# Performance work log

Measured on AMD Instinct MI355X. Metric: run time of the kernel, lower is better.

## Reference

```python
import jax, jax.numpy as jnp
import numpy as np

N_NODES = 50000
N_EDGES = 640000
D_IN = 128
D_OUT = 128


def setup_inputs() -> dict:
    key = jax.random.key(0)
    k1, k2, k3, k4 = jax.random.split(key, 4)
    x = jax.random.normal(k1, (N_NODES, D_IN), dtype=jnp.float32)
    edge_index = jax.random.randint(k2, (2, N_EDGES), 0, N_NODES, dtype=jnp.int64)
    weight = jax.random.uniform(k3, (1,), dtype=jnp.float32)
    temperature = jnp.ones((1,), dtype=jnp.float32)
    W = jax.random.normal(k4, (D_IN, D_OUT), dtype=jnp.float32) * (1.0 / np.sqrt(D_IN))
    b = jnp.zeros((D_OUT,), dtype=jnp.float32)
    return {"x": x, "edge_index": edge_index, "weight": weight,
            "temperature": temperature, "W": W, "b": b}


def _gcn_conv(x, edge_index, W, b):
    N = x.shape[0]
    src, dst = edge_index[0], edge_index[1]
    loop = jnp.arange(N, dtype=edge_index.dtype)
    s = jnp.concatenate([src, loop])  # self-loops appended
    d = jnp.concatenate([dst, loop])
    deg = jax.ops.segment_sum(jnp.ones(s.shape[0], dtype=x.dtype), d, num_segments=N)
    dinv = jnp.where(deg > 0, deg ** -0.5, 0.0)
    norm = dinv[s] * dinv[d]  # [E+N]
    h = x @ W                 # linear transform first (PyG GCNConv)
    msg = h[s] * norm[:, None]
    out = jax.ops.segment_sum(msg, d, num_segments=N)
    return out + b


def _gradient_entropy(x, edge_index, temperature):
    # Boltzmann distribution over per-node Dirichlet energies;
    # entropy gradient w.r.t. node features (computed with autodiff).
    N = x.shape[0]
    src, dst = edge_index[0], edge_index[1]

    def entropy(z):
        diff = z[src] - z[dst]                                  # [E, D]
        E = jax.ops.segment_sum(jnp.sum(diff * diff, axis=-1), dst, num_segments=N)
        logp = jax.nn.log_softmax(-E / temperature[0])
        p = jnp.exp(logp)
        return -jnp.sum(p * logp)

    return jax.grad(entropy)(x)


def reference(x, edge_index, weight, temperature, W, b):
    h = _gcn_conv(x, edge_index, W, b)
    g = jax.lax.stop_gradient(_gradient_entropy(h, edge_index, temperature))
    return h + weight * g
```

## Files before the change

### kernel.cpp

```cpp
#include <hip/hip_runtime.h>

#define N_NODES 50000
#define N_EDGES 640000
#define NSCANB  196
#define MAXD    64

#define OFF_HTMPB    0
#define OFF_OBF      3200000
#define OFF_CURSOR   6400000
#define OFF_E        6450000
#define OFF_PMIN     6500000
#define OFF_PS0      6500256
#define OFF_PS1      6500512
#define OFF_WT       6500768
#define OFF_EBIN     6508960

typedef __attribute__((ext_vector_type(8))) short bf16x8;
typedef __attribute__((ext_vector_type(4))) float f32x4;

__device__ __forceinline__ unsigned short f2bf(float f) {
    unsigned u = __float_as_uint(f);
    unsigned r = u + 0x7fffu + ((u >> 16) & 1u);
    return (unsigned short)(r >> 16);
}
__device__ __forceinline__ float bflo(unsigned u) { return __uint_as_float(u << 16); }
__device__ __forceinline__ float bfhi(unsigned u) { return __uint_as_float(u & 0xffff0000u); }

__global__ __launch_bounds__(256) void k_init(const float* __restrict__ W,
                                              int* __restrict__ cursor,
                                              unsigned short* __restrict__ wtg) {
    int gtid = blockIdx.x * 256 + threadIdx.x;
    if (gtid < N_NODES) cursor[gtid] = 0;
    if (gtid < 4096) {
        int k = gtid >> 5, n4 = (gtid & 31) * 4;
        float4 v = *(const float4*)(W + k * 128 + n4);
        wtg[(n4 + 0) * 128 + k] = f2bf(v.x);
        wtg[(n4 + 1) * 128 + k] = f2bf(v.y);
        wtg[(n4 + 2) * 128 + k] = f2bf(v.z);
        wtg[(n4 + 3) * 128 + k] = f2bf(v.w);
    }
}

__global__ __launch_bounds__(256) void k_gemm(const float* __restrict__ x,
                                              const unsigned short* __restrict__ wtg,
                                              unsigned short* __restrict__ htmpb) {
    int tid = threadIdx.x;
    int wave = tid >> 6, lane = tid & 63, quad = lane >> 4, m16 = lane & 15;
    int r0 = blockIdx.x * 32 + (wave & 1) * 16;
    int ch = (wave >> 1) * 4;
    int arow = r0 + m16;
    int rowc = arow < N_NODES ? arow : N_NODES - 1;
    f32x4 acc[4];
    #pragma unroll
    for (int c = 0; c < 4; c++) acc[c] = (f32x4){0.f, 0.f, 0.f, 0.f};
    #pragma unroll
    for (int kt = 0; kt < 4; kt++) {
        int koff = kt * 32 + quad * 8;
        float4 xa = *(const float4*)(x + rowc * 128 + koff);
        float4 xb = *(const float4*)(x + rowc * 128 + koff + 4);
        bf16x8 af;
        af[0] = (short)f2bf(xa.x); af[1] = (short)f2bf(xa.y);
        af[2] = (short)f2bf(xa.z); af[3] = (short)f2bf(xa.w);
        af[4] = (short)f2bf(xb.x); af[5] = (short)f2bf(xb.y);
        af[6] = (short)f2bf(xb.z); af[7] = (short)f2bf(xb.w);
        #pragma unroll
        for (int c = 0; c < 4; c++) {
            bf16x8 bfrag = *(const bf16x8*)(wtg + ((ch + c) * 16 + m16) * 128 + koff);
            acc[c] = __builtin_amdgcn_mfma_f32_16x16x32_bf16(af, bfrag, acc[c], 0, 0, 0);
        }
    }
    #pragma unroll
    for (int reg = 0; reg < 4; reg++) {
        int grow = r0 + quad * 4 + reg;
        if (grow < N_NODES) {
            #pragma unroll
            for (int c = 0; c < 4; c++)
                htmpb[grow * 128 + (ch + c) * 16 + m16] = f2bf(acc[c][reg]);
        }
    }
}

__global__ __launch_bounds__(256) void k_bucket(const int* __restrict__ src,
                                                const int* __restrict__ dst,
                                                int* __restrict__ cursor,
                                                int* __restrict__ ebin) {
    int e = blockIdx.x * 256 + threadIdx.x;
    int d = dst[e];
    int pos = atomicAdd(&cursor[d], 1);
    if (pos < MAXD) ebin[d * MAXD + pos] = src[e];
}

__global__ __launch_bounds__(256) void k_gather(const unsigned short* __restrict__ htmpb,
                                                const int* __restrict__ deg,
                                                const float* __restrict__ b,
                                                const int* __restrict__ ebin,
                                                float* __restrict__ out,
                                                unsigned short* __restrict__ obf) {
    int node = blockIdx.x * 8 + (threadIdx.x >> 5);
    int lane = threadIdx.x & 31;
    int dg = deg[node]; if (dg > MAXD) dg = MAXD;
    float di = rsqrtf((float)(dg + 1));
    float4 bv = *(const float4*)(b + lane * 4);
    uint2 hv = *(const uint2*)(htmpb + node * 128 + lane * 4);
    float sl = di * di;
    float ax = bv.x + bflo(hv.x) * sl, ay = bv.y + bfhi(hv.x) * sl;
    float az = bv.z + bflo(hv.y) * sl, aw = bv.w + bfhi(hv.y) * sl;
    float cx = 0.f, cy = 0.f, cz = 0.f, cw = 0.f;
    const int* bin = ebin + node * MAXD;
    int k = 0;
    for (; k + 3 < dg; k += 4) {
        int s0 = bin[k], s1 = bin[k + 1], s2 = bin[k + 2], s3 = bin[k + 3];
        float n0 = di * rsqrtf((float)(deg[s0] + 1));
        float n1 = di * rsqrtf((float)(deg[s1] + 1));
        float n2 = di * rsqrtf((float)(deg[s2] + 1));
        float n3 = di * rsqrtf((float)(deg[s3] + 1));
        uint2 u0 = *(const uint2*)(htmpb + s0 * 128 + lane * 4);
        uint2 u1 = *(const uint2*)(htmpb + s1 * 128 + lane * 4);
        uint2 u2 = *(const uint2*)(htmpb + s2 * 128 + lane * 4);
        uint2 u3 = *(const uint2*)(htmpb + s3 * 128 + lane * 4);
        ax += bflo(u0.x) * n0; ay += bfhi(u0.x) * n0;
        az += bflo(u0.y) * n0; aw += bfhi(u0.y) * n0;
        cx += bflo(u1.x) * n1; cy += bfhi(u1.x) * n1;
        cz += bflo(u1.y) * n1; cw += bfhi(u1.y) * n1;
        ax += bflo(u2.x) * n2; ay += bfhi(u2.x) * n2;
        az += bflo(u2.y) * n2; aw += bfhi(u2.y) * n2;
        cx += bflo(u3.x) * n3; cy += bfhi(u3.x) * n3;
        cz += bflo(u3.y) * n3; cw += bfhi(u3.y) * n3;
    }
    for (; k < dg; k++) {
        int s0 = bin[k];
        float n0 = di * rsqrtf((float)(deg[s0] + 1));
        uint2 u0 = *(const uint2*)(htmpb + s0 * 128 + lane * 4);
        ax += bflo(u0.x) * n0; ay += bfhi(u0.x) * n0;
        az += bflo(u0.y) * n0; aw += bfhi(u0.y) * n0;
    }
    ax += cx; ay += cy; az += cz; aw += cw;
    *(float4*)(out + node * 128 + lane * 4) = make_float4(ax, ay, az, aw);
    uint2 pk;
    pk.x = (unsigned)f2bf(ax) | ((unsigned)f2bf(ay) << 16);
    pk.y = (unsigned)f2bf(az) | ((unsigned)f2bf(aw) << 16);
    *(uint2*)(obf + node * 128 + lane * 4) = pk;
}

__global__ __launch_bounds__(256) void k_energy(const unsigned short* __restrict__ obf,
                                                const int* __restrict__ deg,
                                                const int* __restrict__ ebin,
                                                float* __restrict__ E) {
    int node = blockIdx.x * 8 + (threadIdx.x >> 5);
    int lane = threadIdx.x & 31;
    int dg = deg[node]; if (dg > MAXD) dg = MAXD;
    uint2 ud = *(const uint2*)(obf + node * 128 + lane * 4);
    float o0 = bflo(ud.x), o1 = bfhi(ud.x), o2 = bflo(ud.y), o3 = bfhi(ud.y);
    float acc = 0.f, acc2 = 0.f;
    const int* bin = ebin + node * MAXD;
    int k = 0;
    for (; k + 3 < dg; k += 4) {
        int s0 = bin[k], s1 = bin[k + 1], s2 = bin[k + 2], s3 = bin[k + 3];
        uint2 a = *(const uint2*)(obf + s0 * 128 + lane * 4);
        uint2 c = *(const uint2*)(obf + s1 * 128 + lane * 4);
        uint2 g = *(const uint2*)(obf + s2 * 128 + lane * 4);
        uint2 h = *(const uint2*)(obf + s3 * 128 + lane * 4);
        float d0 = bflo(a.x) - o0, d1 = bfhi(a.x) - o1, d2 = bflo(a.y) - o2, d3 = bfhi(a.y) - o3;
        float e4 = bflo(c.x) - o0, e5 = bfhi(c.x) - o1, e6 = bflo(c.y) - o2, e7 = bfhi(c.y) - o3;
        float f0 = bflo(g.x) - o0, f1 = bfhi(g.x) - o1, f2 = bflo(g.y) - o2, f3 = bfhi(g.y) - o3;
        float h4 = bflo(h.x) - o0, h5 = bfhi(h.x) - o1, h6 = bflo(h.y) - o2, h7 = bfhi(h.y) - o3;
        acc  += d0 * d0 + d1 * d1 + d2 * d2 + d3 * d3;
        acc2 += e4 * e4 + e5 * e5 + e6 * e6 + e7 * e7;
        acc  += f0 * f0 + f1 * f1 + f2 * f2 + f3 * f3;
        acc2 += h4 * h4 + h5 * h5 + h6 * h6 + h7 * h7;
    }
    for (; k < dg; k++) {
        int s0 = bin[k];
        uint2 a = *(const uint2*)(obf + s0 * 128 + lane * 4);
        float d0 = bflo(a.x) - o0, d1 = bfhi(a.x) - o1, d2 = bflo(a.y) - o2, d3 = bfhi(a.y) - o3;
        acc += d0 * d0 + d1 * d1 + d2 * d2 + d3 * d3;
    }
    acc += acc2;
    #pragma unroll
    for (int off = 16; off; off >>= 1) acc += __shfl_xor(acc, off);
    if (lane == 0) E[node] = acc;
}

__global__ __launch_bounds__(256) void k_esoft(const float* __restrict__ E,
                                               const float* __restrict__ temp,
                                               float* __restrict__ pmin,
                                               float* __restrict__ ps0,
                                               float* __restrict__ ps1) {
    __shared__ float fred[12];
    int tid = threadIdx.x;
    int i = blockIdx.x * 256 + tid;
    int lane = tid & 63, wid = tid >> 6;
    float e = (i < N_NODES) ? E[i] : 3.402823466e38f;
    float m = e;
    #pragma unroll
    for (int off = 32; off; off >>= 1) m = fminf(m, __shfl_xor(m, off));
    if (lane == 0) fred[wid] = m;
    __syncthreads();
    float bm = fminf(fminf(fred[0], fred[1]), fminf(fred[2], fred[3]));
    float T = temp[0];
    float s0 = 0.f, s1 = 0.f;
    if (i < N_NODES) {
        float dd = (bm - e) / T;
        float ed = __expf(dd);
        s0 = ed; s1 = ed * dd;
    }
    #pragma unroll
    for (int off = 32; off; off >>= 1) { s0 += __shfl_xor(s0, off); s1 += __shfl_xor(s1, off); }
    __syncthreads();
    if (lane == 0) { fred[4 + wid] = s0; fred[8 + wid] = s1; }
    __syncthreads();
    if (tid == 0) {
        pmin[blockIdx.x] = bm;
        ps0[blockIdx.x] = fred[4] + fred[5] + fred[6] + fred[7];
        ps1[blockIdx.x] = fred[8] + fred[9] + fred[10] + fred[11];
    }
}

__global__ __launch_bounds__(256) void k_grad(const int* __restrict__ deg,
                                              const int* __restrict__ ebin,
                                              const float* __restrict__ E,
                                              const float* __restrict__ temp,
                                              const float* __restrict__ pmin,
                                              const float* __restrict__ ps0,
                                              const float* __restrict__ ps1,
                                              const float* __restrict__ weight,
                                              float* __restrict__ out) {
    __shared__ float fred[12];
    int tid = threadIdx.x;
    int lane = tid & 63, wid = tid >> 6;

    float pm = (tid < NSCANB) ? pmin[tid] : 3.402823466e38f;
    float m = pm;
    #pragma unroll
    for (int off = 32; off; off >>= 1) m = fminf(m, __shfl_xor(m, off));
    if (lane == 0) fred[wid] = m;
    __syncthreads();
    float gmin = fminf(fminf(fred[0], fred[1]), fminf(fred[2], fred[3]));
    float T = temp[0];
    float s0 = 0.f, s1 = 0.f;
    if (tid < NSCANB) {
        float dl = (gmin - pm) / T;
        float ex = __expf(dl);
        float b0 = ps0[tid], b1 = ps1[tid];
        s0 = ex * b0;
        s1 = ex * (b1 + dl * b0);
    }
    #pragma unroll
    for (int off = 32; off; off >>= 1) { s0 += __shfl_xor(s0, off); s1 += __shfl_xor(s1, off); }
    __syncthreads();
    if (lane == 0) { fred[4 + wid] = s0; fred[8 + wid] = s1; }
    __syncthreads();
    float S0 = fred[4] + fred[5] + fred[6] + fred[7];
    float S1 = fred[8] + fred[9] + fred[10] + fred[11];

    float wscale = 2.f * weight[0];
    int lane32 = tid & 31;
    int node = blockIdx.x * 8 + (tid >> 5);
    if (node >= N_NODES) return;
    float dd = (gmin - E[node]) / T;
    float qd = (__expf(dd) / S0) * (dd - S1 / S0) / T;
    if (qd == 0.f) return;
    float cc = wscale * qd;
    int dg = deg[node]; if (dg > MAXD) dg = MAXD;
    float4 od = *(const float4*)(out + node * 128 + lane32 * 4);
    float sx = 0.f, sy = 0.f, sz = 0.f, sw = 0.f;
    const int* bin = ebin + node * MAXD;
    for (int k = 0; k < dg; k++) {
        int s = bin[k];
        float4 a = *(const float4*)(out + s * 128 + lane32 * 4);
        float vx = cc * (a.x - od.x), vy = cc * (a.y - od.y);
        float vz = cc * (a.z - od.z), vw = cc * (a.w - od.w);
        float* os = out + s * 128 + lane32 * 4;
        atomicAdd(os + 0, vx); atomicAdd(os + 1, vy);
        atomicAdd(os + 2, vz); atomicAdd(os + 3, vw);
        sx += vx; sy += vy; sz += vz; sw += vw;
    }
    float* odp = out + node * 128 + lane32 * 4;
    atomicAdd(odp + 0, -sx); atomicAdd(odp + 1, -sy);
    atomicAdd(odp + 2, -sz); atomicAdd(odp + 3, -sw);
}

extern "C" void kernel_launch(void* const* d_in, const int* in_sizes, int n_in,
                              void* d_out, int out_size, void* d_ws, size_t ws_size,
                              hipStream_t stream) {
    const float* x      = (const float*)d_in[0];
    const int*   ei     = (const int*)d_in[1];
    const float* weight = (const float*)d_in[2];
    const float* temp   = (const float*)d_in[3];
    const float* W      = (const float*)d_in[4];
    const float* b      = (const float*)d_in[5];
    float* out = (float*)d_out;
    float* ws  = (float*)d_ws;

    const int* src = ei;
    const int* dst = ei + N_EDGES;

    unsigned short* htmpb = (unsigned short*)(ws + OFF_HTMPB);
    unsigned short* obf   = (unsigned short*)(ws + OFF_OBF);
    int*   cursor   = (int*)(ws + OFF_CURSOR);
    float* Earr     = ws + OFF_E;
    float* pminA    = ws + OFF_PMIN;
    float* ps0A     = ws + OFF_PS0;
    float* ps1A     = ws + OFF_PS1;
    unsigned short* wtg = (unsigned short*)(ws + OFF_WT);
    int*   ebin     = (int*)(ws + OFF_EBIN);

    k_init<<<NSCANB, 256, 0, stream>>>(W, cursor, wtg);
    k_gemm<<<1563, 256, 0, stream>>>(x, wtg, htmpb);
    k_bucket<<<N_EDGES / 256, 256, 0, stream>>>(src, dst, cursor, ebin);
    k_gather<<<6250, 256, 0, stream>>>(htmpb, cursor, b, ebin, out, obf);
    k_energy<<<6250, 256, 0, stream>>>(obf, cursor, ebin, Earr);
    k_esoft<<<NSCANB, 256, 0, stream>>>(Earr, temp, pminA, ps0A, ps1A);
    k_grad<<<6250, 256, 0, stream>>>(cursor, ebin, Earr, temp, pminA, ps0A, ps1A, weight, out);
}
```

Before: 218.1 us.

## Fold init into GEMM and fuse softmax statistics into persistent grad kernel

Removes the k_init kernel by zeroing the cursor and converting W to bf16 inside the GEMM, with each lane reading W columns directly (strided fp32 loads) instead of a pre-transposed bf16 copy. Removes k_esoft by having every block of k_grad redundantly compute the global min and online-softmax sums over all 50000 energies, and makes k_grad persistent with 781 blocks in a grid-stride loop. This saves two launches and the intermediate buffers, at the cost of redundant full-array scans per block, uncoalesced W reads in the GEMM, and fewer grad blocks to hide atomic latency.

```diff
diff --git a/kernel.cpp b/kernel.cpp
--- a/kernel.cpp
+++ b/kernel.cpp
@@ -2,18 +2,13 @@
 
 #define N_NODES 50000
 #define N_EDGES 640000
-#define NSCANB  196
 #define MAXD    64
 
 #define OFF_HTMPB    0
 #define OFF_OBF      3200000
 #define OFF_CURSOR   6400000
 #define OFF_E        6450000
-#define OFF_PMIN     6500000
-#define OFF_PS0      6500256
-#define OFF_PS1      6500512
-#define OFF_WT       6500768
-#define OFF_EBIN     6508960
+#define OFF_EBIN     6500000
 
 typedef __attribute__((ext_vector_type(8))) short bf16x8;
 typedef __attribute__((ext_vector_type(4))) float f32x4;
@@ -26,25 +21,14 @@
 __device__ __forceinline__ float bflo(unsigned u) { return __uint_as_float(u << 16); }
 __device__ __forceinline__ float bfhi(unsigned u) { return __uint_as_float(u & 0xffff0000u); }
 
-__global__ __launch_bounds__(256) void k_init(const float* __restrict__ W,
+__global__ __launch_bounds__(256) void k_gemm(const float* __restrict__ x,
+                                              const float* __restrict__ W,
                                               int* __restrict__ cursor,
-                                              unsigned short* __restrict__ wtg) {
-    int gtid = blockIdx.x * 256 + threadIdx.x;
-    if (gtid < N_NODES) cursor[gtid] = 0;
-    if (gtid < 4096) {
-        int k = gtid >> 5, n4 = (gtid & 31) * 4;
-        float4 v = *(const float4*)(W + k * 128 + n4);
-        wtg[(n4 + 0) * 128 + k] = f2bf(v.x);
-        wtg[(n4 + 1) * 128 + k] = f2bf(v.y);
-        wtg[(n4 + 2) * 128 + k] = f2bf(v.z);
-        wtg[(n4 + 3) * 128 + k] = f2bf(v.w);
-    }
-}
-
-__global__ __launch_bounds__(256) void k_gemm(const float* __restrict__ x,
-                                              const unsigned short* __restrict__ wtg,
                                               unsigned short* __restrict__ htmpb) {
     int tid = threadIdx.x;
+    int gtid = blockIdx.x * 256 + tid;
+    if (gtid < N_NODES) cursor[gtid] = 0;
+
     int wave = tid >> 6, lane = tid & 63, quad = lane >> 4, m16 = lane & 15;
     int r0 = blockIdx.x * 32 + (wave & 1) * 16;
     int ch = (wave >> 1) * 4;
@@ -65,7 +49,11 @@
         af[6] = (short)f2bf(xb.z); af[7] = (short)f2bf(xb.w);
         #pragma unroll
         for (int c = 0; c < 4; c++) {
-            bf16x8 bfrag = *(const bf16x8*)(wtg + ((ch + c) * 16 + m16) * 128 + koff);
+            int n = (ch + c) * 16 + m16;
+            bf16x8 bfrag;
+            #pragma unroll
+            for (int j = 0; j < 8; j++)
+                bfrag[j] = (short)f2bf(W[(koff + j) * 128 + n]);
             acc[c] = __builtin_amdgcn_mfma_f32_16x16x32_bf16(af, bfrag, acc[c], 0, 0, 0);
         }
     }
@@ -181,103 +169,82 @@
     if (lane == 0) E[node] = acc;
 }
 
-__global__ __launch_bounds__(256) void k_esoft(const float* __restrict__ E,
-                                               const float* __restrict__ temp,
-                                               float* __restrict__ pmin,
-                                               float* __restrict__ ps0,
-                                               float* __restrict__ ps1) {
-    __shared__ float fred[12];
-    int tid = threadIdx.x;
-    int i = blockIdx.x * 256 + tid;
-    int lane = tid & 63, wid = tid >> 6;
-    float e = (i < N_NODES) ? E[i] : 3.402823466e38f;
-    float m = e;
-    #pragma unroll
-    for (int off = 32; off; off >>= 1) m = fminf(m, __shfl_xor(m, off));
-    if (lane == 0) fred[wid] = m;
-    __syncthreads();
-    float bm = fminf(fminf(fred[0], fred[1]), fminf(fred[2], fred[3]));
-    float T = temp[0];
-    float s0 = 0.f, s1 = 0.f;
-    if (i < N_NODES) {
-        float dd = (bm - e) / T;
-        float ed = __expf(dd);
-        s0 = ed; s1 = ed * dd;
-    }
-    #pragma unroll
-    for (int off = 32; off; off >>= 1) { s0 += __shfl_xor(s0, off); s1 += __shfl_xor(s1, off); }
-    __syncthreads();
-    if (lane == 0) { fred[4 + wid] = s0; fred[8 + wid] = s1; }
-    __syncthreads();
-    if (tid == 0) {
-        pmin[blockIdx.x] = bm;
-        ps0[blockIdx.x] = fred[4] + fred[5] + fred[6] + fred[7];
-        ps1[blockIdx.x] = fred[8] + fred[9] + fred[10] + fred[11];
-    }
-}
-
 __global__ __launch_bounds__(256) void k_grad(const int* __restrict__ deg,
                                               const int* __restrict__ ebin,
                                               const float* __restrict__ E,
                                               const float* __restrict__ temp,
-                                              const float* __restrict__ pmin,
-                                              const float* __restrict__ ps0,
-                                              const float* __restrict__ ps1,
                                               const float* __restrict__ weight,
                                               float* __restrict__ out) {
-    __shared__ float fred[12];
+    __shared__ float sm[4], ss0[4], ss1[4];
     int tid = threadIdx.x;
     int lane = tid & 63, wid = tid >> 6;
-
-    float pm = (tid < NSCANB) ? pmin[tid] : 3.402823466e38f;
-    float m = pm;
-    #pragma unroll
-    for (int off = 32; off; off >>= 1) m = fminf(m, __shfl_xor(m, off));
-    if (lane == 0) fred[wid] = m;
+    float T = temp[0];
+
+    float m = 3.402823466e38f, s0 = 0.f, s1 = 0.f;
+    for (int i = tid; i < N_NODES; i += 256) {
+        float e = E[i];
+        if (e < m) {
+            float d = (e - m) / T;
+            float ex = __expf(d);
+            s1 = ex * (s1 + d * s0);
+            s0 = ex * s0 + 1.f;
+            m = e;
+        } else {
+            float dd = (m - e) / T;
+            float ed = __expf(dd);
+            s0 += ed; s1 += ed * dd;
+        }
+    }
+    #pragma unroll
+    for (int off = 32; off; off >>= 1) {
+        float m2 = __shfl_xor(m, off), t0 = __shfl_xor(s0, off), t1 = __shfl_xor(s1, off);
+        float mn = fminf(m, m2);
+        float da = (mn - m) / T, db = (mn - m2) / T;
+        float ea = __expf(da), eb = __expf(db);
+        float ns0 = ea * s0 + eb * t0;
+        float ns1 = ea * (s1 + da * s0) + eb * (t1 + db * t0);
+        m = mn; s0 = ns0; s1 = ns1;
+    }
+    if (lane == 0) { sm[wid] = m; ss0[wid] = s0; ss1[wid] = s1; }
     __syncthreads();
-    float gmin = fminf(fminf(fred[0], fred[1]), fminf(fred[2], fred[3]));
-    float T = temp[0];
-    float s0 = 0.f, s1 = 0.f;
-    if (tid < NSCANB) {
-        float dl = (gmin - pm) / T;
-        float ex = __expf(dl);
-        float b0 = ps0[tid], b1 = ps1[tid];
-        s0 = ex * b0;
-        s1 = ex * (b1 + dl * b0);
-    }
-    #pragma unroll
-    for (int off = 32; off; off >>= 1) { s0 += __shfl_xor(s0, off); s1 += __shfl_xor(s1, off); }
-    __syncthreads();
-    if (lane == 0) { fred[4 + wid] = s0; fred[8 + wid] = s1; }
-    __syncthreads();
-    float S0 = fred[4] + fred[5] + fred[6] + fred[7];
-    float S1 = fred[8] + fred[9] + fred[10] + fred[11];
+    float gm = sm[0], gs0 = ss0[0], gs1 = ss1[0];
+    #pragma unroll
+    for (int w = 1; w < 4; w++) {
+        float m2 = sm[w], t0 = ss0[w], t1 = ss1[w];
+        float mn = fminf(gm, m2);
+        float da = (mn - gm) / T, db = (mn - m2) / T;
+        float ea = __expf(da), eb = __expf(db);
+        float ns0 = ea * gs0 + eb * t0;
+        float ns1 = ea * (gs1 + da * gs0) + eb * (t1 + db * t0);
+        gm = mn; gs0 = ns0; gs1 = ns1;
+    }
+    float gmin = gm, S0 = gs0, S1 = gs1;
 
     float wscale = 2.f * weight[0];
     int lane32 = tid & 31;
-    int node = blockIdx.x * 8 + (tid >> 5);
-    if (node >= N_NODES) return;
-    float dd = (gmin - E[node]) / T;
-    float qd = (__expf(dd) / S0) * (dd - S1 / S0) / T;
-    if (qd == 0.f) return;
-    float cc = wscale * qd;
-    int dg = deg[node]; if (dg > MAXD) dg = MAXD;
-    float4 od = *(const float4*)(out + node * 128 + lane32 * 4);
-    float sx = 0.f, sy = 0.f, sz = 0.f, sw = 0.f;
-    const int* bin = ebin + node * MAXD;
-    for (int k = 0; k < dg; k++) {
-        int s = bin[k];
-        float4 a = *(const float4*)(out + s * 128 + lane32 * 4);
-        float vx = cc * (a.x - od.x), vy = cc * (a.y - od.y);
-        float vz = cc * (a.z - od.z), vw = cc * (a.w - od.w);
-        float* os = out + s * 128 + lane32 * 4;
-        atomicAdd(os + 0, vx); atomicAdd(os + 1, vy);
-        atomicAdd(os + 2, vz); atomicAdd(os + 3, vw);
-        sx += vx; sy += vy; sz += vz; sw += vw;
-    }
-    float* odp = out + node * 128 + lane32 * 4;
-    atomicAdd(odp + 0, -sx); atomicAdd(odp + 1, -sy);
-    atomicAdd(odp + 2, -sz); atomicAdd(odp + 3, -sw);
+    for (int node = blockIdx.x * 8 + (tid >> 5); node < N_NODES; node += 781 * 8) {
+        float dd = (gmin - E[node]) / T;
+        float qd = (__expf(dd) / S0) * (dd - S1 / S0) / T;
+        if (qd == 0.f) continue;
+        float cc = wscale * qd;
+        int dg = deg[node]; if (dg > MAXD) dg = MAXD;
+        float4 od = *(const float4*)(out + node * 128 + lane32 * 4);
+        float sx = 0.f, sy = 0.f, sz = 0.f, sw = 0.f;
+        const int* bin = ebin + node * MAXD;
+        for (int k = 0; k < dg; k++) {
+            int s = bin[k];
+            float4 a = *(const float4*)(out + s * 128 + lane32 * 4);
+            float vx = cc * (a.x - od.x), vy = cc * (a.y - od.y);
+            float vz = cc * (a.z - od.z), vw = cc * (a.w - od.w);
+            float* os = out + s * 128 + lane32 * 4;
+            atomicAdd(os + 0, vx); atomicAdd(os + 1, vy);
+            atomicAdd(os + 2, vz); atomicAdd(os + 3, vw);
+            sx += vx; sy += vy; sz += vz; sw += vw;
+        }
+        float* odp = out + node * 128 + lane32 * 4;
+        atomicAdd(odp + 0, -sx); atomicAdd(odp + 1, -sy);
+        atomicAdd(odp + 2, -sz); atomicAdd(odp + 3, -sw);
+    }
 }
 
 extern "C" void kernel_launch(void* const* d_in, const int* in_sizes, int n_in,
@@ -299,17 +266,11 @@
     unsigned short* obf   = (unsigned short*)(ws + OFF_OBF);
     int*   cursor   = (int*)(ws + OFF_CURSOR);
     float* Earr     = ws + OFF_E;
-    float* pminA    = ws + OFF_PMIN;
-    float* ps0A     = ws + OFF_PS0;
-    float* ps1A     = ws + OFF_PS1;
-    unsigned short* wtg = (unsigned short*)(ws + OFF_WT);
     int*   ebin     = (int*)(ws + OFF_EBIN);
 
-    k_init<<<NSCANB, 256, 0, stream>>>(W, cursor, wtg);
-    k_gemm<<<1563, 256, 0, stream>>>(x, wtg, htmpb);
+    k_gemm<<<1563, 256, 0, stream>>>(x, W, cursor, htmpb);
     k_bucket<<<N_EDGES / 256, 256, 0, stream>>>(src, dst, cursor, ebin);
     k_gather<<<6250, 256, 0, stream>>>(htmpb, cursor, b, ebin, out, obf);
     k_energy<<<6250, 256, 0, stream>>>(obf, cursor, ebin, Earr);
-    k_esoft<<<NSCANB, 256, 0, stream>>>(Earr, temp, pminA, ps0A, ps1A);
-    k_grad<<<6250, 256, 0, stream>>>(cursor, ebin, Earr, temp, pminA, ps0A, ps1A, weight, out);
-}
+    k_grad<<<781, 256, 0, stream>>>(cursor, ebin, Earr, temp, weight, out);
+}
```

Measured after the change: 277.9 us. 1.27x slower.
